# Kernel tuning notes

Measured on AMD Instinct MI355X. Metric: run time of the kernel, lower is better.

The kernel has to match this reference:

```python
import jax, jax.numpy as jnp
import numpy as np

INPUT_DIM = 1024
HIDDEN_DIM = 64  # per-head dim
NUM_HEADS = 16
LN_EPS = 1e-5


def setup_inputs() -> dict:
    key = jax.random.key(0)
    ks = jax.random.split(key, 12)
    B, S, D = 2, 2048, INPUT_DIM
    HD = HIDDEN_DIM * NUM_HEADS
    s_in = 1.0 / np.sqrt(D)
    s_hd = 1.0 / np.sqrt(HD)
    return {
        "x": jax.random.normal(ks[0], (B, S, D), dtype=jnp.float32),
        "Wq": jax.random.normal(ks[1], (D, HD), dtype=jnp.float32) * s_in,
        "bq": jax.random.normal(ks[2], (HD,), dtype=jnp.float32) * 0.02,
        "Wk": jax.random.normal(ks[3], (D, HD), dtype=jnp.float32) * s_in,
        "bk": jax.random.normal(ks[4], (HD,), dtype=jnp.float32) * 0.02,
        "Wv": jax.random.normal(ks[5], (D, HD), dtype=jnp.float32) * s_in,
        "bv": jax.random.normal(ks[6], (HD,), dtype=jnp.float32) * 0.02,
        "Wo": jax.random.normal(ks[7], (HD, D), dtype=jnp.float32) * s_hd,
        "bo": jax.random.normal(ks[8], (D,), dtype=jnp.float32) * 0.02,
        "gamma": jnp.ones((D,), dtype=jnp.float32),
        "beta": jnp.zeros((D,), dtype=jnp.float32),
    }


def _layer_norm(y, gamma, beta):
    mu = jnp.mean(y, axis=-1, keepdims=True)
    var = jnp.mean(jnp.square(y - mu), axis=-1, keepdims=True)
    return (y - mu) * jax.lax.rsqrt(var + LN_EPS) * gamma + beta


def reference(x, Wq, bq, Wk, bk, Wv, bv, Wo, bo, gamma, beta):
    B, S, D = x.shape
    H, Hd = NUM_HEADS, HIDDEN_DIM
    # Faithful to the torch module: (B,S,H*Hd) -> reshape (B,H,S,Hd) WITHOUT transpose.
    Q = (x @ Wq + bq).reshape(B, H, S, Hd)
    K = (x @ Wk + bk).reshape(B, H, S, Hd)
    V = (x @ Wv + bv).reshape(B, H, S, Hd)
    scores = jnp.einsum("bhqd,bhkd->bhqk", Q, K) / jnp.sqrt(jnp.float32(Hd))
    attn = jax.nn.softmax(scores, axis=-1)  # dropout=0 -> identity
    ctx = jnp.einsum("bhqk,bhkd->bhqd", attn, V).reshape(B, S, H * Hd)
    out = _layer_norm(x + (ctx @ Wo + bo), gamma, beta)
    return jax.nn.gelu(out, approximate=False)
```

## Files before the change

### kernel.cpp

```cpp
#include <hip/hip_runtime.h>
#include <hip/hip_bf16.h>
#include <cstdint>
#include <cstddef>


#define SEQ   2048
#define DIM   1024
#define NHEAD 16
#define HDIM  64
#define ROWS  4096

#define QSCALE 0.1803368801111204f

typedef __attribute__((ext_vector_type(8))) __bf16 bf16x8;
typedef __attribute__((ext_vector_type(4))) float floatx4;
typedef __attribute__((ext_vector_type(8))) unsigned short ushortx8;

__device__ __forceinline__ unsigned short f2bf(float f) {
  unsigned int u = __float_as_uint(f);
  u += 0x7FFFu + ((u >> 16) & 1u);
  return (unsigned short)(u >> 16);
}

__device__ __forceinline__ unsigned int pk2bf(float a, float b) {
  float2 f; f.x = a; f.y = b;
  __hip_bfloat162 h = __float22bfloat162_rn(f);
  return *(unsigned int*)&h;
}

__device__ __forceinline__ void glds16(const unsigned short* g,
                                       unsigned short* l) {
  __builtin_amdgcn_global_load_lds(
      (const __attribute__((address_space(1))) void*)g,
      (__attribute__((address_space(3))) void*)l, 16, 0, 0);
}

__global__ __launch_bounds__(256) void prep_all(
    const float* __restrict__ x,
    const float* __restrict__ Wq, const float* __restrict__ Wk,
    const float* __restrict__ Wv, const float* __restrict__ Wo,
    unsigned short* __restrict__ xb,
    unsigned short* __restrict__ Wqkvt, unsigned short* __restrict__ Wot) {
  __shared__ float t[32][33];
  const int z = blockIdx.z;
  const int tx = threadIdx.x, ty = threadIdx.y;
  if (z == 4) {
    const int bid = blockIdx.y * 32 + blockIdx.x;
    const int tid = ty * 32 + tx;
#pragma unroll
    for (int p = 0; p < 4; ++p) {
      const int i = bid * 1024 + p * 256 + tid;
      float4 v = ((const float4*)x)[i];
      ushort4 o;
      o.x = f2bf(v.x); o.y = f2bf(v.y); o.z = f2bf(v.z); o.w = f2bf(v.w);
      ((ushort4*)xb)[i] = o;
    }
    return;
  }
  const float* in = (z == 0) ? Wq : (z == 1) ? Wk : (z == 2) ? Wv : Wo;
  unsigned short* out = (z < 3) ? Wqkvt + (size_t)z * DIM * DIM : Wot;
  const int bx = blockIdx.x * 32, by = blockIdx.y * 32;
#pragma unroll
  for (int i = ty; i < 32; i += 8)
    t[i][tx] = in[(size_t)(by + i) * DIM + bx + tx];
  __syncthreads();
#pragma unroll
  for (int i = ty; i < 32; i += 8)
    out[(size_t)(bx + i) * DIM + by + tx] = f2bf(t[tx][i]);
}

__global__ __launch_bounds__(256) void swizzle_kv(
    unsigned short* __restrict__ Kb,
    const unsigned short* __restrict__ Vb,
    unsigned short* __restrict__ Vs) {
  __shared__ unsigned short t[64 * 72];
  const int tile = blockIdx.x;
  const int bh   = blockIdx.y;
  const int isV  = blockIdx.z;
  const int tid  = threadIdx.x;
  const size_t base = (size_t)bh * (SEQ * HDIM) + (size_t)tile * 4096;
  const unsigned short* src = (isV ? Vb : Kb) + base;
#pragma unroll
  for (int p = 0; p < 2; ++p) {
    const int c = p * 256 + tid;
    *(ushortx8*)&t[(c >> 3) * 72 + (c & 7) * 8] = *(const ushortx8*)&src[c * 8];
  }
  __syncthreads();
  unsigned short* dst = (isV ? Vs : Kb) + base;
  const int lane = tid & 63, wave = tid >> 6;
  const int l16 = lane & 15, quad = lane >> 4;
  if (!isV) {
#pragma unroll
    for (int p = 0; p < 2; ++p) {
      const int f = wave * 2 + p;
      const int step = f >> 2, g = f & 3;
      *(ushortx8*)&dst[f * 512 + lane * 8] =
          *(const ushortx8*)&t[(g * 16 + l16) * 72 + step * 32 + quad * 8];
    }
  } else {
#pragma unroll
    for (int p = 0; p < 2; ++p) {
      const int f = wave * 2 + p;
      const int step = f >> 2, g = f & 3;
      ushortx8 v;
#pragma unroll
      for (int e = 0; e < 8; ++e)
        v[e] = t[(step * 32 + quad * 8 + e) * 72 + g * 16 + l16];
      *(ushortx8*)&dst[f * 512 + lane * 8] = v;
    }
  }
}

__global__ __launch_bounds__(256, 3) void gemm_qkv(
    const unsigned short* __restrict__ A,
    const unsigned short* __restrict__ Wt,
    const float* __restrict__ bq, const float* __restrict__ bk,
    const float* __restrict__ bv,
    unsigned short* __restrict__ Qb, unsigned short* __restrict__ Kb,
    unsigned short* __restrict__ Vb) {
  constexpr int K = DIM;
  __shared__ unsigned short As[128 * 64];
  __shared__ unsigned short Bs[128 * 64];
  const int tid  = threadIdx.x;
  const int lane = tid & 63, wave = tid >> 6;
  const int l16  = lane & 15, quad = lane >> 4;
  const int wm   = (wave & 1) * 64, wn = (wave >> 1) * 64;
  const int tm   = blockIdx.y * 128, tn = blockIdx.x * 128;
  const int grow = lane >> 3, gcol = (lane & 7) * 8;

  floatx4 acc[4][4] = {};

  for (int k0 = 0; k0 < K; k0 += 64) {
    __syncthreads();
#pragma unroll
    for (int p = 0; p < 4; ++p) {
      const int q = wave * 4 + p;
      const int row = q * 8 + grow;
      glds16(&A [(size_t)(tm + row) * K + k0 + gcol], &As[q * 512]);
      glds16(&Wt[(size_t)(tn + row) * K + k0 + gcol], &Bs[q * 512]);
    }
    __syncthreads();
#pragma unroll
    for (int step = 0; step < 2; ++step) {
      const int kk = step * 32 + quad * 8;
      bf16x8 af[4], bfr[4];
#pragma unroll
      for (int i = 0; i < 4; ++i)
        af[i] = *(const bf16x8*)&As[(wm + i * 16 + l16) * 64 + kk];
#pragma unroll
      for (int j = 0; j < 4; ++j)
        bfr[j] = *(const bf16x8*)&Bs[(wn + j * 16 + l16) * 64 + kk];
#pragma unroll
      for (int i = 0; i < 4; ++i)
#pragma unroll
        for (int j = 0; j < 4; ++j)
          acc[i][j] = __builtin_amdgcn_mfma_f32_16x16x32_bf16(af[i], bfr[j],
                                                              acc[i][j], 0, 0, 0);
    }
  }

#pragma unroll
  for (int j = 0; j < 4; ++j) {
    const int ng  = tn + wn + j * 16 + l16;
    const int seg = ng >> 10;
    const int col = ng & 1023;
    const float* bp    = (seg == 0) ? bq : (seg == 1) ? bk : bv;
    unsigned short* op = (seg == 0) ? Qb : (seg == 1) ? Kb : Vb;
    const float bias = bp[col];
    const float scl  = (seg == 0) ? QSCALE : 1.0f;
#pragma unroll
    for (int i = 0; i < 4; ++i) {
      const int m0 = tm + wm + i * 16 + quad * 4;
#pragma unroll
      for (int r = 0; r < 4; ++r)
        op[(size_t)(m0 + r) * DIM + col] = f2bf((acc[i][j][r] + bias) * scl);
    }
  }
}

__global__ __launch_bounds__(256) void gemm_o(
    const unsigned short* __restrict__ A,
    const unsigned short* __restrict__ Wt,
    const float* __restrict__ bo,
    float* __restrict__ Y) {
  constexpr int K = DIM;
  __shared__ unsigned short As[128 * 64];
  __shared__ unsigned short Bs[64 * 64];
  const int tid  = threadIdx.x;
  const int lane = tid & 63, wave = tid >> 6;
  const int l16  = lane & 15, quad = lane >> 4;
  const int wm   = wave * 32;
  const int tm   = blockIdx.y * 128, tn = blockIdx.x * 64;
  const int grow = lane >> 3, gcol = (lane & 7) * 8;

  floatx4 acc[2][4] = {};

  for (int k0 = 0; k0 < K; k0 += 64) {
    __syncthreads();
#pragma unroll
    for (int p = 0; p < 4; ++p) {
      const int q = wave * 4 + p;
      const int row = q * 8 + grow;
      glds16(&A[(size_t)(tm + row) * K + k0 + gcol], &As[q * 512]);
    }
#pragma unroll
    for (int p = 0; p < 2; ++p) {
      const int q = wave * 2 + p;
      const int row = q * 8 + grow;
      glds16(&Wt[(size_t)(tn + row) * K + k0 + gcol], &Bs[q * 512]);
    }
    __syncthreads();
#pragma unroll
    for (int step = 0; step < 2; ++step) {
      const int kk = step * 32 + quad * 8;
      bf16x8 af[2], bfr[4];
#pragma unroll
      for (int i = 0; i < 2; ++i)
        af[i] = *(const bf16x8*)&As[(wm + i * 16 + l16) * 64 + kk];
#pragma unroll
      for (int j = 0; j < 4; ++j)
        bfr[j] = *(const bf16x8*)&Bs[(j * 16 + l16) * 64 + kk];
#pragma unroll
      for (int i = 0; i < 2; ++i)
#pragma unroll
        for (int j = 0; j < 4; ++j)
          acc[i][j] = __builtin_amdgcn_mfma_f32_16x16x32_bf16(af[i], bfr[j],
                                                              acc[i][j], 0, 0, 0);
    }
  }

#pragma unroll
  for (int j = 0; j < 4; ++j) {
    const int n = tn + j * 16 + l16;
    const float bias = bo[n];
#pragma unroll
    for (int i = 0; i < 2; ++i) {
      const int m0 = tm + wm + i * 16 + quad * 4;
#pragma unroll
      for (int r = 0; r < 4; ++r)
        Y[(size_t)(m0 + r) * DIM + n] = acc[i][j][r] + bias;
    }
  }
}

__global__ __launch_bounds__(256) void attn_fwd(
    const unsigned short* __restrict__ Qb,
    const unsigned short* __restrict__ Ks,
    const unsigned short* __restrict__ Vs,
    unsigned short* __restrict__ ctx) {
  __shared__ unsigned short Pl[4][32 * 72];

  const int tid  = threadIdx.x;
  const int lane = tid & 63, wave = tid >> 6;
  const int l16  = lane & 15, quad = lane >> 4;
  const int id   = blockIdx.x;
  const int w    = id >> 3;
  const int head = (id & 7) * 4 + (w & 3);
  const int qt   = w >> 2;
  const size_t slab = (size_t)head * SEQ * HDIM;
  const unsigned short* Q  = Qb + slab;
  const unsigned short* Kf = Ks + slab;
  const unsigned short* Vf = Vs + slab;
  const int q0 = qt * 32;

  bf16x8 qf[2][2];
#pragma unroll
  for (int h = 0; h < 2; ++h) {
    qf[h][0] = *(const bf16x8*)&Q[(size_t)(q0 + h * 16 + l16) * HDIM + quad * 8];
    qf[h][1] = *(const bf16x8*)&Q[(size_t)(q0 + h * 16 + l16) * HDIM + 32 + quad * 8];
  }

  floatx4 o[2][4] = {};
  float lr[2] = {0.f, 0.f};

  for (int t = 0; t < 8; ++t) {
    const int tile = wave * 8 + t;
    const unsigned short* kb = Kf + (size_t)tile * 4096;
    const unsigned short* vb = Vf + (size_t)tile * 4096;
    bf16x8 kf[2][4], vf[2][4];
#pragma unroll
    for (int step = 0; step < 2; ++step)
#pragma unroll
      for (int g = 0; g < 4; ++g) {
        kf[step][g] = *(const bf16x8*)&kb[(step * 4 + g) * 512 + lane * 8];
        vf[step][g] = *(const bf16x8*)&vb[(step * 4 + g) * 512 + lane * 8];
      }

    floatx4 s[2][4] = {};
#pragma unroll
    for (int step = 0; step < 2; ++step)
#pragma unroll
      for (int mt = 0; mt < 4; ++mt) {
        s[0][mt] = __builtin_amdgcn_mfma_f32_16x16x32_bf16(kf[step][mt], qf[0][step], s[0][mt], 0, 0, 0);
        s[1][mt] = __builtin_amdgcn_mfma_f32_16x16x32_bf16(kf[step][mt], qf[1][step], s[1][mt], 0, 0, 0);
      }

#pragma unroll
    for (int h = 0; h < 2; ++h) {
#pragma unroll
      for (int mt = 0; mt < 4; ++mt) {
        float p0 = __builtin_amdgcn_exp2f(s[h][mt][0]);
        float p1 = __builtin_amdgcn_exp2f(s[h][mt][1]);
        float p2 = __builtin_amdgcn_exp2f(s[h][mt][2]);
        float p3 = __builtin_amdgcn_exp2f(s[h][mt][3]);
        lr[h] += (p0 + p1) + (p2 + p3);
        uint2 pv;
        pv.x = pk2bf(p0, p1);
        pv.y = pk2bf(p2, p3);
        *(uint2*)&Pl[wave][(h * 16 + l16) * 72 + mt * 16 + quad * 4] = pv;
      }
    }
    __asm__ __volatile__("s_waitcnt lgkmcnt(0)" ::: "memory");

#pragma unroll
    for (int step = 0; step < 2; ++step) {
      const int kk = step * 32 + quad * 8;
      bf16x8 pf0 = *(const bf16x8*)&Pl[wave][(l16) * 72 + kk];
      bf16x8 pf1 = *(const bf16x8*)&Pl[wave][(16 + l16) * 72 + kk];
#pragma unroll
      for (int j = 0; j < 4; ++j) {
        o[0][j] = __builtin_amdgcn_mfma_f32_16x16x32_bf16(pf0, vf[step][j], o[0][j], 0, 0, 0);
        o[1][j] = __builtin_amdgcn_mfma_f32_16x16x32_bf16(pf1, vf[step][j], o[1][j], 0, 0, 0);
      }
    }
  }

#pragma unroll
  for (int h = 0; h < 2; ++h) {
    lr[h] += __shfl_xor(lr[h], 16, 64);
    lr[h] += __shfl_xor(lr[h], 32, 64);
  }

  if (wave != 0) {
#pragma unroll
    for (int h = 0; h < 2; ++h) {
      if (quad == 0)
        *(float*)&Pl[wave][2048 + 2 * (h * 16 + l16)] = lr[h];
#pragma unroll
      for (int j = 0; j < 4; ++j)
#pragma unroll
        for (int r = 0; r < 4; ++r)
          Pl[wave][(h * 16 + quad * 4 + r) * 64 + j * 16 + l16] =
              f2bf(o[h][j][r]);
    }
  }
  __syncthreads();

  if (wave == 0) {
    unsigned short* cp = ctx + slab;
#pragma unroll
    for (int h = 0; h < 2; ++h) {
      float lt = lr[h];
#pragma unroll
      for (int p = 1; p < 4; ++p)
        lt += *(const float*)&Pl[p][2048 + 2 * (h * 16 + l16)];
      float lb[4];
#pragma unroll
      for (int r = 0; r < 4; ++r)
        lb[r] = 1.0f / __shfl(lt, quad * 4 + r, 64);
#pragma unroll
      for (int j = 0; j < 4; ++j)
#pragma unroll
        for (int r = 0; r < 4; ++r) {
          const int row = h * 16 + quad * 4 + r;
          float v = o[h][j][r];
#pragma unroll
          for (int p = 1; p < 4; ++p)
            v += __uint_as_float(
                (unsigned int)Pl[p][row * 64 + j * 16 + l16] << 16);
          cp[(size_t)(q0 + row) * HDIM + j * 16 + l16] = f2bf(v * lb[r]);
        }
    }
  }
}

__global__ __launch_bounds__(256) void ln_gelu(
    const float* __restrict__ x, const float* __restrict__ y,
    const float* __restrict__ gamma, const float* __restrict__ beta,
    float* __restrict__ out) {
  const int row = blockIdx.x;
  const int tid = threadIdx.x;
  const float4 xv = ((const float4*)(x + (size_t)row * DIM))[tid];
  const float4 yv = ((const float4*)(y + (size_t)row * DIM))[tid];
  float4 s;
  s.x = xv.x + yv.x; s.y = xv.y + yv.y; s.z = xv.z + yv.z; s.w = xv.w + yv.w;
  float sum = (s.x + s.y) + (s.z + s.w);
  float sq  = (s.x * s.x + s.y * s.y) + (s.z * s.z + s.w * s.w);
#pragma unroll
  for (int off = 1; off < 64; off <<= 1) {
    sum += __shfl_xor(sum, off, 64);
    sq  += __shfl_xor(sq, off, 64);
  }
  __shared__ float red[8];
  const int wave = tid >> 6, lane = tid & 63;
  if (lane == 0) { red[wave] = sum; red[wave + 4] = sq; }
  __syncthreads();
  sum = red[0] + red[1] + red[2] + red[3];
  sq  = red[4] + red[5] + red[6] + red[7];
  const float mu   = sum * (1.0f / DIM);
  const float var  = sq * (1.0f / DIM) - mu * mu;
  const float rstd = rsqrtf(var + 1e-5f);
  const float4 gv = ((const float4*)gamma)[tid];
  const float4 bv = ((const float4*)beta)[tid];
  float4 ov;
  {
    const float v = (s.x - mu) * rstd * gv.x + bv.x;
    ov.x = 0.5f * v * (1.0f + erff(v * 0.70710678118654752f));
  }
  {
    const float v = (s.y - mu) * rstd * gv.y + bv.y;
    ov.y = 0.5f * v * (1.0f + erff(v * 0.70710678118654752f));
  }
  {
    const float v = (s.z - mu) * rstd * gv.z + bv.z;
    ov.z = 0.5f * v * (1.0f + erff(v * 0.70710678118654752f));
  }
  {
    const float v = (s.w - mu) * rstd * gv.w + bv.w;
    ov.w = 0.5f * v * (1.0f + erff(v * 0.70710678118654752f));
  }
  ((float4*)(out + (size_t)row * DIM))[tid] = ov;
}

extern "C" void kernel_launch(void* const* d_in, const int* in_sizes, int n_in,
                              void* d_out, int out_size, void* d_ws, size_t ws_size,
                              hipStream_t stream) {
  (void)in_sizes; (void)n_in; (void)out_size; (void)ws_size;
  const float* x     = (const float*)d_in[0];
  const float* Wq    = (const float*)d_in[1];
  const float* bq    = (const float*)d_in[2];
  const float* Wk    = (const float*)d_in[3];
  const float* bk    = (const float*)d_in[4];
  const float* Wv    = (const float*)d_in[5];
  const float* bv    = (const float*)d_in[6];
  const float* Wo    = (const float*)d_in[7];
  const float* bo    = (const float*)d_in[8];
  const float* gamma = (const float*)d_in[9];
  const float* beta  = (const float*)d_in[10];
  float* out = (float*)d_out;

  char* ws = (char*)d_ws;
  const size_t MB = 1u << 20;
  unsigned short* xb    = (unsigned short*)(ws);
  unsigned short* Wqkvt = (unsigned short*)(ws + 8 * MB);
  unsigned short* Wot   = (unsigned short*)(ws + 14 * MB);
  unsigned short* Qb    = (unsigned short*)(ws + 16 * MB);
  unsigned short* Kb    = (unsigned short*)(ws + 24 * MB);
  unsigned short* Vs    = (unsigned short*)(ws + 32 * MB);
  unsigned short* Vb    = (unsigned short*)(ws + 40 * MB);
  unsigned short* Cx    = (unsigned short*)(ws + 40 * MB);
  float*          Y     = (float*)(ws + 48 * MB);

  prep_all<<<dim3(32, 32, 5), dim3(32, 8), 0, stream>>>(x, Wq, Wk, Wv, Wo,
                                                        xb, Wqkvt, Wot);
  gemm_qkv<<<dim3(24, 32), 256, 0, stream>>>(xb, Wqkvt, bq, bk, bv, Qb, Kb, Vb);
  swizzle_kv<<<dim3(SEQ / 64, 32, 2), 256, 0, stream>>>(Kb, Vb, Vs);
  attn_fwd<<<2048, 256, 0, stream>>>(Qb, Kb, Vs, Cx);
  gemm_o<<<dim3(16, 32), 256, 0, stream>>>(Cx, Wot, bo, Y);
  ln_gelu<<<ROWS, 256, 0, stream>>>(x, Y, gamma, beta, out);
}
```

Before: 218.6 us.

## Split attention block work into 2 query tiles by 2 key halves

Each attention block now handles 64 query rows with waves arranged as two query sub-tiles times two key halves, instead of 32 query rows with four waves each taking a quarter of the keys. The grid is halved and each wave iterates twice as many key tiles. The final merge now combines only pairs of partial outputs and is spread across all 256 threads with vectorized stores, rather than serialized on wave 0. This cuts cross-wave reduction cost and per-block overhead but reduces the number of blocks, which may lower occupancy or latency hiding.

```diff
diff --git a/kernel.cpp b/kernel.cpp
--- a/kernel.cpp
+++ b/kernel.cpp
@@ -253,15 +253,16 @@
   const int tid  = threadIdx.x;
   const int lane = tid & 63, wave = tid >> 6;
   const int l16  = lane & 15, quad = lane >> 4;
+  const int wq   = wave >> 1, wk = wave & 1;
   const int id   = blockIdx.x;
   const int w    = id >> 3;
   const int head = (id & 7) * 4 + (w & 3);
-  const int qt   = w >> 2;
+  const int qp   = w >> 2;
   const size_t slab = (size_t)head * SEQ * HDIM;
   const unsigned short* Q  = Qb + slab;
   const unsigned short* Kf = Ks + slab;
   const unsigned short* Vf = Vs + slab;
-  const int q0 = qt * 32;
+  const int q0 = qp * 64 + wq * 32;
 
   bf16x8 qf[2][2];
 #pragma unroll
@@ -273,8 +274,8 @@
   floatx4 o[2][4] = {};
   float lr[2] = {0.f, 0.f};
 
-  for (int t = 0; t < 8; ++t) {
-    const int tile = wave * 8 + t;
+  for (int t = 0; t < 16; ++t) {
+    const int tile = wk * 16 + t;
     const unsigned short* kb = Kf + (size_t)tile * 4096;
     const unsigned short* vb = Vf + (size_t)tile * 4096;
     bf16x8 kf[2][4], vf[2][4];
@@ -331,45 +332,39 @@
     lr[h] += __shfl_xor(lr[h], 32, 64);
   }
 
-  if (wave != 0) {
-#pragma unroll
-    for (int h = 0; h < 2; ++h) {
-      if (quad == 0)
-        *(float*)&Pl[wave][2048 + 2 * (h * 16 + l16)] = lr[h];
-#pragma unroll
-      for (int j = 0; j < 4; ++j)
-#pragma unroll
-        for (int r = 0; r < 4; ++r)
-          Pl[wave][(h * 16 + quad * 4 + r) * 64 + j * 16 + l16] =
-              f2bf(o[h][j][r]);
-    }
+#pragma unroll
+  for (int h = 0; h < 2; ++h) {
+    if (quad == 0)
+      *(float*)&Pl[wave][2048 + 2 * (h * 16 + l16)] = lr[h];
+#pragma unroll
+    for (int j = 0; j < 4; ++j)
+#pragma unroll
+      for (int r = 0; r < 4; ++r)
+        Pl[wave][(h * 16 + quad * 4 + r) * 64 + j * 16 + l16] =
+            f2bf(o[h][j][r]);
   }
   __syncthreads();
 
-  if (wave == 0) {
-    unsigned short* cp = ctx + slab;
-#pragma unroll
-    for (int h = 0; h < 2; ++h) {
-      float lt = lr[h];
-#pragma unroll
-      for (int p = 1; p < 4; ++p)
-        lt += *(const float*)&Pl[p][2048 + 2 * (h * 16 + l16)];
-      float lb[4];
-#pragma unroll
-      for (int r = 0; r < 4; ++r)
-        lb[r] = 1.0f / __shfl(lt, quad * 4 + r, 64);
-#pragma unroll
-      for (int j = 0; j < 4; ++j)
-#pragma unroll
-        for (int r = 0; r < 4; ++r) {
-          const int row = h * 16 + quad * 4 + r;
-          float v = o[h][j][r];
-#pragma unroll
-          for (int p = 1; p < 4; ++p)
-            v += __uint_as_float(
-                (unsigned int)Pl[p][row * 64 + j * 16 + l16] << 16);
-          cp[(size_t)(q0 + row) * HDIM + j * 16 + l16] = f2bf(v * lb[r]);
-        }
+  {
+    const int g = tid >> 7, u = tid & 127;
+    const int q = u >> 2, d0 = (u & 3) * 16;
+    const int sa = g * 2, sb = g * 2 + 1;
+    const float lt = *(const float*)&Pl[sa][2048 + 2 * q] +
+                     *(const float*)&Pl[sb][2048 + 2 * q];
+    const float inv = 1.0f / lt;
+    unsigned short* cp = ctx + slab + (size_t)(qp * 64 + g * 32 + q) * HDIM;
+#pragma unroll
+    for (int c = 0; c < 2; ++c) {
+      ushortx8 a = *(const ushortx8*)&Pl[sa][q * 64 + d0 + c * 8];
+      ushortx8 b = *(const ushortx8*)&Pl[sb][q * 64 + d0 + c * 8];
+      ushortx8 ov;
+#pragma unroll
+      for (int e = 0; e < 8; ++e) {
+        const float fa = __uint_as_float((unsigned int)a[e] << 16);
+        const float fb = __uint_as_float((unsigned int)b[e] << 16);
+        ov[e] = f2bf((fa + fb) * inv);
+      }
+      *(ushortx8*)&cp[d0 + c * 8] = ov;
     }
   }
 }
@@ -455,7 +450,7 @@
                                                         xb, Wqkvt, Wot);
   gemm_qkv<<<dim3(24, 32), 256, 0, stream>>>(xb, Wqkvt, bq, bk, bv, Qb, Kb, Vb);
   swizzle_kv<<<dim3(SEQ / 64, 32, 2), 256, 0, stream>>>(Kb, Vb, Vs);
-  attn_fwd<<<2048, 256, 0, stream>>>(Qb, Kb, Vs, Cx);
+  attn_fwd<<<1024, 256, 0, stream>>>(Qb, Kb, Vs, Cx);
   gemm_o<<<dim3(16, 32), 256, 0, stream>>>(Cx, Wot, bo, Y);
   ln_gelu<<<ROWS, 256, 0, stream>>>(x, Y, gamma, beta, out);
 }
```

Result: faster. 214.0 us, median of 2 (-2.1%).
